# Optimization experiments

Hardware: AMD Instinct MI355X
Metric: run time of the kernel (lower is better)

The kernel has to match this reference:

```python
import jax, jax.numpy as jnp
import numpy as np
from jax import lax


def _quadrature_weights(bw):
    # s2cnn-style Driscoll-Healy quadrature weights over beta, length 2*bw
    j = np.arange(2 * bw)
    k = np.arange(bw)
    theta = np.pi * (2 * j + 1) / (4 * bw)
    s = (np.sin(np.outer(2 * j + 1, 2 * k + 1) * np.pi / (4 * bw)) / (2 * k + 1)).sum(-1)
    return jnp.asarray((2.0 / bw) * np.sin(theta) * s, jnp.float32)


def _conv2d(x, W, b):
    y = lax.conv_general_dilated(x, W, (1, 1), 'SAME',
                                 dimension_numbers=('NCHW', 'OIHW', 'NCHW'))
    return y + b[None, :, None, None]


def setup_inputs() -> dict:
    key = jax.random.key(0)
    ks = jax.random.split(key, 8)
    b, n = 8, 32768
    res_pt, res_r = 32, 8
    inputs = jax.random.normal(ks[0], (b, n, 3), jnp.float32)
    return {
        'inputs': inputs,
        'scale': jnp.float32(3.0),      # max radius covered by radial bins
        'sigma': jnp.float32(0.5),      # gaussian width in grid units
        'A': jnp.float32(1.0),          # splat amplitude
        'inteval_comp': jnp.float32(0.5),
        'res_pt': res_pt,
        'res_r': res_r,
        'W_s2_1': 0.08 * jax.random.normal(ks[1], (32, 8, 3, 3), jnp.float32),
        'b_s2_1': jnp.zeros((32,), jnp.float32),
        'W_s2_2': 0.05 * jax.random.normal(ks[2], (64, 32, 3, 3), jnp.float32),
        'b_s2_2': jnp.zeros((64,), jnp.float32),
        'W_gamma': 0.1 * jax.random.normal(ks[3], (64, 32), jnp.float32),
        'W_c3_1': 0.05 * jax.random.normal(ks[4], (64, 128), jnp.float32),
        'b_c3_1': jnp.zeros((64,), jnp.float32),
        'W_c3_2': 0.05 * jax.random.normal(ks[5], (32, 64), jnp.float32),
        'b_c3_2': jnp.zeros((32,), jnp.float32),
    }


def reference(inputs, scale, sigma, A, inteval_comp, res_pt, res_r,
              W_s2_1, b_s2_1, W_s2_2, b_s2_2, W_gamma,
              W_c3_1, b_c3_1, W_c3_2, b_c3_2):
    b, n, _ = inputs.shape
    # ---- remap: cartesian -> spherical with min-radius clamp (utils.remap) ----
    x, y, z = inputs[..., 0], inputs[..., 1], inputs[..., 2]
    r = jnp.maximum(jnp.sqrt(x * x + y * y + z * z), 0.1)
    theta = jnp.arccos(jnp.clip(z / r, -1.0, 1.0))            # [0, pi]
    phi = jnp.arctan2(y, x) + np.pi                            # [0, 2pi)
    # ---- s2_gridding: gaussian-weighted point -> (theta,phi,r) grid scatter ----
    ct = theta / np.pi * res_pt                                # continuous bin coords
    cp = phi / (2 * np.pi) * res_pt
    cr = r / scale * res_r
    it = jnp.clip(jnp.floor(ct).astype(jnp.int32), 0, res_pt - 1)
    ip = jnp.clip(jnp.floor(cp).astype(jnp.int32), 0, res_pt - 1)
    ir = jnp.clip(jnp.floor(cr).astype(jnp.int32), 0, res_r - 1)
    d2 = ((ct - (it + inteval_comp)) ** 2
          + (cp - (ip + inteval_comp)) ** 2
          + (cr - (ir + inteval_comp)) ** 2)
    w = A * jnp.exp(-d2 / (2.0 * sigma * sigma))               # (b, n)
    vals = jnp.stack([w, w * x, w * y, w * z], axis=-1)        # (b, n, 4)
    bidx = jnp.arange(b, dtype=jnp.int32)[:, None] * jnp.ones((1, n), jnp.int32)
    flat = ((bidx * res_pt + it) * res_pt + ip) * res_r + ir   # (b, n)
    grid = jnp.zeros((b * res_pt * res_pt * res_r, 4), jnp.float32)
    grid = grid.at[flat.reshape(-1)].add(vals.reshape(-1, 4))
    grid = grid.reshape(b, res_pt, res_pt, res_r, 4)
    ft = jnp.transpose(grid[..., 0], (0, 3, 1, 2))             # (b, res_r, res_pt, res_pt)
    # ---- encoder_l1 (s2cnn_equators): S2 convs + gamma lift to SO3 grid ----
    h = jax.nn.relu(_conv2d(ft, W_s2_1, b_s2_1))
    h = jax.nn.relu(_conv2d(h, W_s2_2, b_s2_2))                # (b, 64, res_pt, res_pt)
    ft_grid = jnp.einsum('bcxy,cg->bcxyg', h, W_gamma)         # (b, 64, rp, rp, rp)
    # ---- so3_integrate: quadrature weight over beta, sum alpha/gamma ----
    wq = _quadrature_weights(res_pt // 2)                      # (res_pt,)
    ft_max = jnp.einsum('bcxyg,y->bc', ft_grid, wq)            # (b, 64)
    # ---- broadcast global feature, concat, pointwise conv3d head ----
    ft_max_ = jnp.broadcast_to(ft_max[:, :, None, None, None],
                               (b, ft_grid.shape[1], res_pt, res_pt, res_pt))
    cat = jnp.concatenate([ft_grid, ft_max_], axis=1)          # (b, 128, rp, rp, rp)
    h3 = jax.nn.relu(jnp.einsum('bcxyg,dc->bdxyg', cat, W_c3_1)
                     + b_c3_1[None, :, None, None, None])
    out = (jnp.einsum('bdxyg,ed->bexyg', h3, W_c3_2)
           + b_c3_2[None, :, None, None, None])                # (b, 32, rp, rp, rp)
    ft_g = out.reshape(b, out.shape[1], -1).max(-1)            # (b, 32)
    return (out, ft_g)
```

## Files before the change

### kernel.cpp

```cpp
#include <hip/hip_runtime.h>
#include <math.h>

#define PI_D 3.14159265358979323846
#define PI_F 3.14159265358979323846f

typedef _Float16 half8 __attribute__((ext_vector_type(8)));
typedef _Float16 half2v __attribute__((ext_vector_type(2)));
typedef float floatx4 __attribute__((ext_vector_type(4)));
#define MFMA16(a,b,c) __builtin_amdgcn_mfma_f32_16x16x32_f16(a,b,c,0,0,0)

__global__ void k_scatter(const float* __restrict__ inp,
                          const float* __restrict__ p_scale,
                          const float* __restrict__ p_sigma,
                          const float* __restrict__ p_A,
                          const float* __restrict__ p_ic,
                          float* __restrict__ ft) {
  int i = blockIdx.x * 256 + threadIdx.x;
  float scale = p_scale[0];
  float sigma = p_sigma[0];
  float A     = p_A[0];
  float icomp = p_ic[0];
  int b = i >> 15;
  float x = inp[i*3+0];
  float y = inp[i*3+1];
  float z = inp[i*3+2];
  float r = sqrtf(x*x + y*y + z*z);
  r = fmaxf(r, 0.1f);
  float ctv = fminf(fmaxf(z / r, -1.0f), 1.0f);
  float theta = acosf(ctv);
  float phi = atan2f(y, x) + PI_F;
  float ct = theta * (32.0f / PI_F);
  float cp = phi * (32.0f / (2.0f * PI_F));
  float cr = r / scale * 8.0f;
  int it = (int)floorf(ct); it = min(max(it, 0), 31);
  int ip = (int)floorf(cp); ip = min(max(ip, 0), 31);
  int ir = (int)floorf(cr); ir = min(max(ir, 0), 7);
  float dt = ct - ((float)it + icomp);
  float dp = cp - ((float)ip + icomp);
  float dr = cr - ((float)ir + icomp);
  float d2 = dt*dt + dp*dp + dr*dr;
  float w = A * expf(-d2 / (2.0f * sigma * sigma));
  atomicAdd(&ft[((b*8 + ir)*32 + it)*32 + ip], w);
}

__global__ void k_wq(float* __restrict__ wq) {
  int t = threadIdx.x;
  double jj = 2.0*(double)t + 1.0;
  double theta = PI_D * jj / 64.0;
  double s = 0.0;
  for (int k = 0; k < 16; ++k)
    s += sin(jj * (double)(2*k+1) * PI_D / 64.0) / (double)(2*k+1);
  wq[t] = (float)((2.0/16.0) * sin(theta) * s);
}

__global__ void k_prepV(const float* __restrict__ Wg, const float* __restrict__ Wc31,
                        _Float16* __restrict__ VswH, _Float16* __restrict__ VswL) {
  int flat = blockIdx.x * 256 + threadIdx.x;
  int jj = flat & 7;
  int l  = (flat >> 3) & 63;
  int rest = flat >> 9;
  int ks = rest & 1, mt = rest >> 1;
  int c = ks*32 + (l >> 4)*8 + jj;
  int m = mt*16 + (l & 15);
  int g = m >> 6, d = m & 63;
  float val = Wg[c*32 + g] * Wc31[d*128 + c];
  _Float16 hi = (_Float16)val;
  _Float16 lo = (_Float16)(val - (float)hi);
  VswH[flat] = hi;
  VswL[flat] = lo;
}

__global__ void k_prepW2(const float* __restrict__ Wc32,
                         _Float16* __restrict__ W2swH, _Float16* __restrict__ W2swL) {
  int flat = blockIdx.x * 256 + threadIdx.x;
  int jj = flat & 7;
  int l  = (flat >> 3) & 63;
  int rest = flat >> 9;
  int ks = rest & 1, mt2 = rest >> 1;
  int e = mt2*16 + (l & 15);
  int d = ks*32 + (l >> 4)*8 + jj;
  float val = Wc32[e*64 + d];
  _Float16 hi = (_Float16)val;
  _Float16 lo = (_Float16)(val - (float)hi);
  W2swH[flat] = hi;
  W2swL[flat] = lo;
}

__global__ void k_conv1(const float* __restrict__ ft, const float* __restrict__ W,
                        const float* __restrict__ bias, float* __restrict__ h1) {
  int blk = blockIdx.x;
  int b = blk >> 5, oc = blk & 31;
  __shared__ float Ws[72];
  int t = threadIdx.x;
  if (t < 72) Ws[t] = W[oc*72 + t];
  __syncthreads();
  int x = t >> 5, y = t & 31;
  float acc = bias[oc];
  const float* fb = ft + b*8192;
  for (int ic = 0; ic < 8; ++ic) {
    const float* fc = fb + ic*1024;
    const float* wr = Ws + ic*9;
#pragma unroll
    for (int dx = -1; dx <= 1; ++dx) {
      int xx = x + dx;
      bool okx = ((unsigned)xx < 32u);
#pragma unroll
      for (int dy = -1; dy <= 1; ++dy) {
        int yy = y + dy;
        float v = (okx && ((unsigned)yy < 32u)) ? fc[xx*32 + yy] : 0.f;
        acc = fmaf(v, wr[(dx+1)*3 + (dy+1)], acc);
      }
    }
  }
  h1[(b*32 + oc)*1024 + t] = fmaxf(acc, 0.f);
}

__global__ __launch_bounds__(512) void k_conv2(const float* __restrict__ h1,
                        const float* __restrict__ W,
                        const float* __restrict__ bias, float* __restrict__ h2) {
  int blk = blockIdx.x;
  int b = blk >> 5, q = blk & 31;
  int oc0 = (q >> 1) * 4, xh = q & 1;
  __shared__ float Ws[4*288];
  int t = threadIdx.x;
  for (int idx = t; idx < 4*288; idx += 512) Ws[idx] = W[oc0*288 + idx];
  __syncthreads();
  int x = xh*16 + (t >> 5), y = t & 31;
  float a0 = bias[oc0+0], a1 = bias[oc0+1], a2 = bias[oc0+2], a3 = bias[oc0+3];
  const float* hb = h1 + b*32*1024;
  for (int ic = 0; ic < 32; ++ic) {
    const float* hc = hb + ic*1024;
    const float* w0 = Ws + 0*288 + ic*9;
    const float* w1 = Ws + 1*288 + ic*9;
    const float* w2 = Ws + 2*288 + ic*9;
    const float* w3 = Ws + 3*288 + ic*9;
#pragma unroll
    for (int dx = -1; dx <= 1; ++dx) {
      int xx = x + dx;
      bool okx = ((unsigned)xx < 32u);
#pragma unroll
      for (int dy = -1; dy <= 1; ++dy) {
        int yy = y + dy;
        float v = (okx && ((unsigned)yy < 32u)) ? hc[xx*32 + yy] : 0.f;
        int k = (dx+1)*3 + (dy+1);
        a0 = fmaf(v, w0[k], a0);
        a1 = fmaf(v, w1[k], a1);
        a2 = fmaf(v, w2[k], a2);
        a3 = fmaf(v, w3[k], a3);
      }
    }
  }
  int p = x*32 + y;
  h2[(b*64 + oc0+0)*1024 + p] = fmaxf(a0, 0.f);
  h2[(b*64 + oc0+1)*1024 + p] = fmaxf(a1, 0.f);
  h2[(b*64 + oc0+2)*1024 + p] = fmaxf(a2, 0.f);
  h2[(b*64 + oc0+3)*1024 + p] = fmaxf(a3, 0.f);
}

__global__ void k_reduce(const float* __restrict__ h2, const float* __restrict__ Wg,
                         const float* __restrict__ wq, float* __restrict__ ftmax) {
  int blk = blockIdx.x;
  int b = blk >> 6, c = blk & 63;
  __shared__ float wqs[32];
  __shared__ float red[256];
  int t = threadIdx.x;
  if (t < 32) wqs[t] = wq[t];
  __syncthreads();
  const float* hb = h2 + (b*64 + c)*1024;
  float acc = 0.f;
  for (int i = t; i < 1024; i += 256) acc = fmaf(hb[i], wqs[i & 31], acc);
  red[t] = acc;
  __syncthreads();
  for (int s2 = 128; s2 > 0; s2 >>= 1) {
    if (t < s2) red[t] += red[t + s2];
    __syncthreads();
  }
  if (t == 0) {
    float sg = 0.f;
    for (int g = 0; g < 32; ++g) sg += Wg[c*32 + g];
    ftmax[b*64 + c] = sg * red[0];
  }
}

__global__ __launch_bounds__(512) void k_head(
    const float* __restrict__ h2, const float* __restrict__ ftmax,
    const float* __restrict__ Wc31, const float* __restrict__ bc31,
    const float* __restrict__ bc32,
    const half8* __restrict__ VswH, const half8* __restrict__ VswL,
    const half8* __restrict__ W2swH, const half8* __restrict__ W2swL,
    float* __restrict__ out, float* __restrict__ blockmax) {
  __shared__ __align__(16) _Float16 h3H[512*72];
  __shared__ __align__(16) _Float16 h3L[512*72];
  __shared__ __align__(16) _Float16 h2H[32*72];
  __shared__ __align__(16) _Float16 h2L[32*72];
  __shared__ float Ks[64];
  __shared__ float vbuf2[8*16];
  int blk = blockIdx.x;
  int b = blk >> 5, x = blk & 31;
  int t = threadIdx.x;
  int lane = t & 63, w = t >> 6;
  int n16 = lane & 15, quad = lane >> 4;

  for (int idx = t; idx < 2048; idx += 512) {
    int c = idx & 63, y = idx >> 6;
    float v = h2[(b*64 + c)*1024 + x*32 + y];
    _Float16 hi = (_Float16)v;
    h2H[y*72 + c] = hi;
    h2L[y*72 + c] = (_Float16)(v - (float)hi);
  }
  if (t < 64) {
    float acc = bc31[t];
    for (int c = 0; c < 64; ++c)
      acc = fmaf(Wc31[t*128 + 64 + c], ftmax[b*64 + c], acc);
    Ks[t] = acc;
  }
  __syncthreads();

  half8 bh00, bh01, bh10, bh11, bl00, bl01, bl10, bl11;
  {
    int a00 = (0*16 + n16)*72 + 0*32 + quad*8;
    int a01 = (0*16 + n16)*72 + 1*32 + quad*8;
    int a10 = (1*16 + n16)*72 + 0*32 + quad*8;
    int a11 = (1*16 + n16)*72 + 1*32 + quad*8;
    bh00 = *(const half8*)&h2H[a00];  bl00 = *(const half8*)&h2L[a00];
    bh01 = *(const half8*)&h2H[a01];  bl01 = *(const half8*)&h2L[a01];
    bh10 = *(const half8*)&h2H[a10];  bl10 = *(const half8*)&h2L[a10];
    bh11 = *(const half8*)&h2H[a11];  bl11 = *(const half8*)&h2L[a11];
  }
  int mt2 = w & 1;
  half8 a2h0 = W2swH[(mt2*2 + 0)*64 + lane];
  half8 a2h1 = W2swH[(mt2*2 + 1)*64 + lane];
  half8 a2l0 = W2swL[(mt2*2 + 0)*64 + lane];
  half8 a2l1 = W2swL[(mt2*2 + 1)*64 + lane];
  float bias_e[4];
#pragma unroll
  for (int r = 0; r < 4; ++r) bias_e[r] = bc32[mt2*16 + quad*4 + r];

  float vmax[4] = {-3.4e38f, -3.4e38f, -3.4e38f, -3.4e38f};

  for (int h = 0; h < 2; ++h) {
    if (h) __syncthreads();
    for (int i = 0; i < 8; ++i) {
      int mt = h*64 + w*8 + i;
      half8 ah0 = VswH[(mt*2 + 0)*64 + lane];
      half8 ah1 = VswH[(mt*2 + 1)*64 + lane];
      half8 al0 = VswL[(mt*2 + 0)*64 + lane];
      half8 al1 = VswL[(mt*2 + 1)*64 + lane];
      floatx4 acc0 = {0.f, 0.f, 0.f, 0.f};
      floatx4 acc1 = {0.f, 0.f, 0.f, 0.f};
      acc0 = MFMA16(ah0, bh00, acc0);  acc1 = MFMA16(ah0, bh10, acc1);
      acc0 = MFMA16(ah0, bl00, acc0);  acc1 = MFMA16(ah0, bl10, acc1);
      acc0 = MFMA16(al0, bh00, acc0);  acc1 = MFMA16(al0, bh10, acc1);
      acc0 = MFMA16(ah1, bh01, acc0);  acc1 = MFMA16(ah1, bh11, acc1);
      acc0 = MFMA16(ah1, bl01, acc0);  acc1 = MFMA16(ah1, bl11, acc1);
      acc0 = MFMA16(al1, bh01, acc0);  acc1 = MFMA16(al1, bh11, acc1);
      int g = mt >> 2, gl = g & 15;
      int dbase = (mt & 3)*16 + quad*4;
      float4 kv = *(const float4*)&Ks[dbase];
#pragma unroll
      for (int nt = 0; nt < 2; ++nt) {
        floatx4 a = nt ? acc1 : acc0;
        int y = nt*16 + n16;
        int rowc = y*16 + gl;
        int dsw = (dbase + y*8) & 63;
        float v0 = fmaxf(a[0] + kv.x, 0.f);
        float v1 = fmaxf(a[1] + kv.y, 0.f);
        float v2 = fmaxf(a[2] + kv.z, 0.f);
        float v3 = fmaxf(a[3] + kv.w, 0.f);
        _Float16 c0 = (_Float16)v0, c1 = (_Float16)v1, c2 = (_Float16)v2, c3 = (_Float16)v3;
        half2v hh0 = {c0, c1}, hh1 = {c2, c3};
        half2v ll0 = {(_Float16)(v0 - (float)c0), (_Float16)(v1 - (float)c1)};
        half2v ll1 = {(_Float16)(v2 - (float)c2), (_Float16)(v3 - (float)c3)};
        int base = rowc*72 + dsw;
        *(half2v*)&h3H[base]     = hh0;
        *(half2v*)&h3H[base + 2] = hh1;
        *(half2v*)&h3L[base]     = ll0;
        *(half2v*)&h3L[base + 2] = ll1;
      }
    }
    __syncthreads();
    for (int i = 0; i < 8; ++i) {
      int nt2 = (w >> 1)*8 + i;
      int rowc = nt2*16 + n16;
      floatx4 acc = {0.f, 0.f, 0.f, 0.f};
      {
        int dsw0 = (0*32 + quad*8 + nt2*8) & 63;
        int dsw1 = (1*32 + quad*8 + nt2*8) & 63;
        half8 b2h0 = *(const half8*)&h3H[rowc*72 + dsw0];
        half8 b2l0 = *(const half8*)&h3L[rowc*72 + dsw0];
        half8 b2h1 = *(const half8*)&h3H[rowc*72 + dsw1];
        half8 b2l1 = *(const half8*)&h3L[rowc*72 + dsw1];
        acc = MFMA16(a2h0, b2h0, acc);
        acc = MFMA16(a2h0, b2l0, acc);
        acc = MFMA16(a2l0, b2h0, acc);
        acc = MFMA16(a2h1, b2h1, acc);
        acc = MFMA16(a2h1, b2l1, acc);
        acc = MFMA16(a2l1, b2h1, acc);
      }
      int y = nt2, g = h*16 + n16;
      size_t base = (((size_t)(b*32 + mt2*16 + quad*4))*1024 + (size_t)(x*32 + y))*32 + g;
#pragma unroll
      for (int r = 0; r < 4; ++r) {
        float v = acc[r] + bias_e[r];
        out[base + (size_t)r*32768] = v;
        vmax[r] = fmaxf(vmax[r], v);
      }
    }
  }
#pragma unroll
  for (int m = 1; m < 16; m <<= 1) {
#pragma unroll
    for (int r = 0; r < 4; ++r)
      vmax[r] = fmaxf(vmax[r], __shfl_xor(vmax[r], m, 64));
  }
  if (n16 == 0) {
#pragma unroll
    for (int r = 0; r < 4; ++r) vbuf2[w*16 + quad*4 + r] = vmax[r];
  }
  __syncthreads();
  if (t < 32) {
    int e = t, m2 = e >> 4, el = e & 15;
    float mm = fmaxf(fmaxf(vbuf2[(m2+0)*16 + el], vbuf2[(m2+2)*16 + el]),
                     fmaxf(vbuf2[(m2+4)*16 + el], vbuf2[(m2+6)*16 + el]));
    blockmax[blk*32 + e] = mm;
  }
}

__global__ void k_final(const float* __restrict__ blockmax, float* __restrict__ ftg) {
  int t = threadIdx.x;
  int b = t >> 5, e = t & 31;
  float m = -3.4e38f;
  for (int x = 0; x < 32; ++x) m = fmaxf(m, blockmax[(b*32 + x)*32 + e]);
  ftg[b*32 + e] = m;
}

extern "C" void kernel_launch(void* const* d_in, const int* in_sizes, int n_in,
                              void* d_out, int out_size, void* d_ws, size_t ws_size,
                              hipStream_t stream) {
  const float* inputs = (const float*)d_in[0];
  const float* scale  = (const float*)d_in[1];
  const float* sigma  = (const float*)d_in[2];
  const float* A      = (const float*)d_in[3];
  const float* icmp   = (const float*)d_in[4];
  const float* W1   = (const float*)d_in[7];
  const float* b1   = (const float*)d_in[8];
  const float* W2   = (const float*)d_in[9];
  const float* b2   = (const float*)d_in[10];
  const float* Wg   = (const float*)d_in[11];
  const float* Wc31 = (const float*)d_in[12];
  const float* bc31 = (const float*)d_in[13];
  const float* Wc32 = (const float*)d_in[14];
  const float* bc32 = (const float*)d_in[15];

  float* ws    = (float*)d_ws;
  float* ft    = ws;
  float* h1    = ws + 65536;
  float* h2    = ws + 327680;
  float* ftmax = ws + 851968;
  float* bmax  = ws + 852480;
  float* wq    = ws + 860672;
  _Float16* VswH  = (_Float16*)(ws + 860704);
  _Float16* VswL  = (_Float16*)(ws + 926240);
  _Float16* W2swH = (_Float16*)(ws + 991776);
  _Float16* W2swL = (_Float16*)(ws + 992800);
  float* out   = (float*)d_out;
  float* ftg   = out + 8388608;

  hipMemsetAsync(ft, 0, 65536*sizeof(float), stream);
  k_wq<<<1, 32, 0, stream>>>(wq);
  k_prepV<<<512, 256, 0, stream>>>(Wg, Wc31, VswH, VswL);
  k_prepW2<<<8, 256, 0, stream>>>(Wc32, W2swH, W2swL);
  k_scatter<<<1024, 256, 0, stream>>>(inputs, scale, sigma, A, icmp, ft);
  k_conv1<<<256, 1024, 0, stream>>>(ft, W1, b1, h1);
  k_conv2<<<256, 512, 0, stream>>>(h1, W2, b2, h2);
  k_reduce<<<512, 256, 0, stream>>>(h2, Wg, wq, ftmax);
  k_head<<<256, 512, 0, stream>>>(h2, ftmax, Wc31, bc31, bc32,
                                  (const half8*)VswH, (const half8*)VswL,
                                  (const half8*)W2swH, (const half8*)W2swL,
                                  out, bmax);
  k_final<<<1, 256, 0, stream>>>(bmax, ftg);
}
```

Measured before the change: 179.8 us.

## Fuse all stages into one cooperative persistent kernel with grid syncs

Replaces the memset and nine separate kernel launches with a single cooperative kernel of 256 blocks that runs every stage in sequence, separated by grid-wide barriers. Shared memory is one byte buffer that each stage reinterprets. The goal is to remove per-launch overhead and the idle gaps between dependent small kernels. In exchange, each stage is limited to 256 blocks, so conv1, the scatter and the reduce each do more work per thread. Each grid.sync has its own cost, and the large shared allocation limits occupancy for every phase.

Result: slower. 332.3 us (+84.8%).

```diff
diff --git a/kernel.cpp b/kernel.cpp
--- a/kernel.cpp
+++ b/kernel.cpp
@@ -1,5 +1,8 @@
 #include <hip/hip_runtime.h>
+#include <hip/hip_cooperative_groups.h>
 #include <math.h>
+
+namespace cg = cooperative_groups;
 
 #define PI_D 3.14159265358979323846
 #define PI_F 3.14159265358979323846f
@@ -9,374 +12,369 @@
 typedef float floatx4 __attribute__((ext_vector_type(4)));
 #define MFMA16(a,b,c) __builtin_amdgcn_mfma_f32_16x16x32_f16(a,b,c,0,0,0)
 
-__global__ void k_scatter(const float* __restrict__ inp,
-                          const float* __restrict__ p_scale,
-                          const float* __restrict__ p_sigma,
-                          const float* __restrict__ p_A,
-                          const float* __restrict__ p_ic,
-                          float* __restrict__ ft) {
-  int i = blockIdx.x * 256 + threadIdx.x;
-  float scale = p_scale[0];
-  float sigma = p_sigma[0];
-  float A     = p_A[0];
-  float icomp = p_ic[0];
-  int b = i >> 15;
-  float x = inp[i*3+0];
-  float y = inp[i*3+1];
-  float z = inp[i*3+2];
-  float r = sqrtf(x*x + y*y + z*z);
-  r = fmaxf(r, 0.1f);
-  float ctv = fminf(fmaxf(z / r, -1.0f), 1.0f);
-  float theta = acosf(ctv);
-  float phi = atan2f(y, x) + PI_F;
-  float ct = theta * (32.0f / PI_F);
-  float cp = phi * (32.0f / (2.0f * PI_F));
-  float cr = r / scale * 8.0f;
-  int it = (int)floorf(ct); it = min(max(it, 0), 31);
-  int ip = (int)floorf(cp); ip = min(max(ip, 0), 31);
-  int ir = (int)floorf(cr); ir = min(max(ir, 0), 7);
-  float dt = ct - ((float)it + icomp);
-  float dp = cp - ((float)ip + icomp);
-  float dr = cr - ((float)ir + icomp);
-  float d2 = dt*dt + dp*dp + dr*dr;
-  float w = A * expf(-d2 / (2.0f * sigma * sigma));
-  atomicAdd(&ft[((b*8 + ir)*32 + it)*32 + ip], w);
-}
-
-__global__ void k_wq(float* __restrict__ wq) {
-  int t = threadIdx.x;
-  double jj = 2.0*(double)t + 1.0;
-  double theta = PI_D * jj / 64.0;
-  double s = 0.0;
-  for (int k = 0; k < 16; ++k)
-    s += sin(jj * (double)(2*k+1) * PI_D / 64.0) / (double)(2*k+1);
-  wq[t] = (float)((2.0/16.0) * sin(theta) * s);
-}
-
-__global__ void k_prepV(const float* __restrict__ Wg, const float* __restrict__ Wc31,
-                        _Float16* __restrict__ VswH, _Float16* __restrict__ VswL) {
-  int flat = blockIdx.x * 256 + threadIdx.x;
-  int jj = flat & 7;
-  int l  = (flat >> 3) & 63;
-  int rest = flat >> 9;
-  int ks = rest & 1, mt = rest >> 1;
-  int c = ks*32 + (l >> 4)*8 + jj;
-  int m = mt*16 + (l & 15);
-  int g = m >> 6, d = m & 63;
-  float val = Wg[c*32 + g] * Wc31[d*128 + c];
-  _Float16 hi = (_Float16)val;
-  _Float16 lo = (_Float16)(val - (float)hi);
-  VswH[flat] = hi;
-  VswL[flat] = lo;
-}
-
-__global__ void k_prepW2(const float* __restrict__ Wc32,
-                         _Float16* __restrict__ W2swH, _Float16* __restrict__ W2swL) {
-  int flat = blockIdx.x * 256 + threadIdx.x;
-  int jj = flat & 7;
-  int l  = (flat >> 3) & 63;
-  int rest = flat >> 9;
-  int ks = rest & 1, mt2 = rest >> 1;
-  int e = mt2*16 + (l & 15);
-  int d = ks*32 + (l >> 4)*8 + jj;
-  float val = Wc32[e*64 + d];
-  _Float16 hi = (_Float16)val;
-  _Float16 lo = (_Float16)(val - (float)hi);
-  W2swH[flat] = hi;
-  W2swL[flat] = lo;
-}
-
-__global__ void k_conv1(const float* __restrict__ ft, const float* __restrict__ W,
-                        const float* __restrict__ bias, float* __restrict__ h1) {
-  int blk = blockIdx.x;
-  int b = blk >> 5, oc = blk & 31;
-  __shared__ float Ws[72];
-  int t = threadIdx.x;
-  if (t < 72) Ws[t] = W[oc*72 + t];
-  __syncthreads();
-  int x = t >> 5, y = t & 31;
-  float acc = bias[oc];
-  const float* fb = ft + b*8192;
-  for (int ic = 0; ic < 8; ++ic) {
-    const float* fc = fb + ic*1024;
-    const float* wr = Ws + ic*9;
-#pragma unroll
-    for (int dx = -1; dx <= 1; ++dx) {
-      int xx = x + dx;
-      bool okx = ((unsigned)xx < 32u);
-#pragma unroll
-      for (int dy = -1; dy <= 1; ++dy) {
-        int yy = y + dy;
-        float v = (okx && ((unsigned)yy < 32u)) ? fc[xx*32 + yy] : 0.f;
-        acc = fmaf(v, wr[(dx+1)*3 + (dy+1)], acc);
+struct KParams {
+  const float *inp, *scale, *sigma, *A, *icmp;
+  const float *W1, *b1, *W2, *b2, *Wg, *Wc31, *bc31, *Wc32, *bc32;
+  float *ft, *h1, *h2, *ftmax, *bmax, *wq;
+  _Float16 *VswH, *VswL, *W2swH, *W2swL;
+  float *out, *ftg;
+};
+
+__global__ __launch_bounds__(512, 2) void k_main(KParams p) {
+  __shared__ __align__(16) char smem[157440];
+  cg::grid_group grid = cg::this_grid();
+  const int blk = blockIdx.x;
+  const int t = threadIdx.x;
+
+  {
+    int flat = blk * 512 + t;
+    {
+      int jj = flat & 7;
+      int l  = (flat >> 3) & 63;
+      int rest = flat >> 9;
+      int ks = rest & 1, mt = rest >> 1;
+      int c = ks*32 + (l >> 4)*8 + jj;
+      int m = mt*16 + (l & 15);
+      int g = m >> 6, d = m & 63;
+      float val = p.Wg[c*32 + g] * p.Wc31[d*128 + c];
+      _Float16 hi = (_Float16)val;
+      p.VswH[flat] = hi;
+      p.VswL[flat] = (_Float16)(val - (float)hi);
+    }
+    if (flat < 2048) {
+      int jj = flat & 7;
+      int l  = (flat >> 3) & 63;
+      int rest = flat >> 9;
+      int ks = rest & 1, mt2 = rest >> 1;
+      int e = mt2*16 + (l & 15);
+      int d = ks*32 + (l >> 4)*8 + jj;
+      float val = p.Wc32[e*64 + d];
+      _Float16 hi = (_Float16)val;
+      p.W2swH[flat] = hi;
+      p.W2swL[flat] = (_Float16)(val - (float)hi);
+    }
+    if (flat < 16384) ((float4*)p.ft)[flat] = make_float4(0.f, 0.f, 0.f, 0.f);
+    if (blk == 255 && t < 32) {
+      double jj = 2.0*(double)t + 1.0;
+      double theta = PI_D * jj / 64.0;
+      double s = 0.0;
+      for (int k = 0; k < 16; ++k)
+        s += sin(jj * (double)(2*k+1) * PI_D / 64.0) / (double)(2*k+1);
+      p.wq[t] = (float)((2.0/16.0) * sin(theta) * s);
+    }
+  }
+  grid.sync();
+
+  {
+    float scale = p.scale[0], sigma = p.sigma[0], A = p.A[0], icomp = p.icmp[0];
+#pragma unroll
+    for (int ii = 0; ii < 2; ++ii) {
+      int i = blk * 512 + t + ii * 131072;
+      int b = i >> 15;
+      float x = p.inp[i*3+0];
+      float y = p.inp[i*3+1];
+      float z = p.inp[i*3+2];
+      float r = sqrtf(x*x + y*y + z*z);
+      r = fmaxf(r, 0.1f);
+      float ctv = fminf(fmaxf(z / r, -1.0f), 1.0f);
+      float theta = acosf(ctv);
+      float phi = atan2f(y, x) + PI_F;
+      float ct = theta * (32.0f / PI_F);
+      float cp = phi * (32.0f / (2.0f * PI_F));
+      float cr = r / scale * 8.0f;
+      int it = (int)floorf(ct); it = min(max(it, 0), 31);
+      int ip = (int)floorf(cp); ip = min(max(ip, 0), 31);
+      int ir = (int)floorf(cr); ir = min(max(ir, 0), 7);
+      float dt = ct - ((float)it + icomp);
+      float dp = cp - ((float)ip + icomp);
+      float dr = cr - ((float)ir + icomp);
+      float d2 = dt*dt + dp*dp + dr*dr;
+      float w = A * expf(-d2 / (2.0f * sigma * sigma));
+      atomicAdd(&p.ft[((b*8 + ir)*32 + it)*32 + ip], w);
+    }
+  }
+  grid.sync();
+
+  {
+    int b = blk >> 5, oc = blk & 31;
+    float* Ws = (float*)smem;
+    if (t < 72) Ws[t] = p.W1[oc*72 + t];
+    __syncthreads();
+    const float* fb = p.ft + b*8192;
+    float bias = p.b1[oc];
+#pragma unroll
+    for (int pp = 0; pp < 2; ++pp) {
+      int px = t + pp*512;
+      int x = px >> 5, y = px & 31;
+      float acc = bias;
+      for (int ic = 0; ic < 8; ++ic) {
+        const float* fc = fb + ic*1024;
+        const float* wr = Ws + ic*9;
+#pragma unroll
+        for (int dx = -1; dx <= 1; ++dx) {
+          int xx = x + dx;
+          bool okx = ((unsigned)xx < 32u);
+#pragma unroll
+          for (int dy = -1; dy <= 1; ++dy) {
+            int yy = y + dy;
+            float v = (okx && ((unsigned)yy < 32u)) ? fc[xx*32 + yy] : 0.f;
+            acc = fmaf(v, wr[(dx+1)*3 + (dy+1)], acc);
+          }
+        }
       }
-    }
-  }
-  h1[(b*32 + oc)*1024 + t] = fmaxf(acc, 0.f);
-}
-
-__global__ __launch_bounds__(512) void k_conv2(const float* __restrict__ h1,
-                        const float* __restrict__ W,
-                        const float* __restrict__ bias, float* __restrict__ h2) {
-  int blk = blockIdx.x;
-  int b = blk >> 5, q = blk & 31;
-  int oc0 = (q >> 1) * 4, xh = q & 1;
-  __shared__ float Ws[4*288];
-  int t = threadIdx.x;
-  for (int idx = t; idx < 4*288; idx += 512) Ws[idx] = W[oc0*288 + idx];
-  __syncthreads();
-  int x = xh*16 + (t >> 5), y = t & 31;
-  float a0 = bias[oc0+0], a1 = bias[oc0+1], a2 = bias[oc0+2], a3 = bias[oc0+3];
-  const float* hb = h1 + b*32*1024;
-  for (int ic = 0; ic < 32; ++ic) {
-    const float* hc = hb + ic*1024;
-    const float* w0 = Ws + 0*288 + ic*9;
-    const float* w1 = Ws + 1*288 + ic*9;
-    const float* w2 = Ws + 2*288 + ic*9;
-    const float* w3 = Ws + 3*288 + ic*9;
-#pragma unroll
-    for (int dx = -1; dx <= 1; ++dx) {
-      int xx = x + dx;
-      bool okx = ((unsigned)xx < 32u);
-#pragma unroll
-      for (int dy = -1; dy <= 1; ++dy) {
-        int yy = y + dy;
-        float v = (okx && ((unsigned)yy < 32u)) ? hc[xx*32 + yy] : 0.f;
-        int k = (dx+1)*3 + (dy+1);
-        a0 = fmaf(v, w0[k], a0);
-        a1 = fmaf(v, w1[k], a1);
-        a2 = fmaf(v, w2[k], a2);
-        a3 = fmaf(v, w3[k], a3);
+      p.h1[(b*32 + oc)*1024 + px] = fmaxf(acc, 0.f);
+    }
+  }
+  grid.sync();
+
+  {
+    int b = blk >> 5, q = blk & 31;
+    int oc0 = (q >> 1) * 4, xh = q & 1;
+    float* Ws = (float*)smem;
+    for (int idx = t; idx < 4*288; idx += 512) Ws[idx] = p.W2[oc0*288 + idx];
+    __syncthreads();
+    int x = xh*16 + (t >> 5), y = t & 31;
+    float a0 = p.b2[oc0+0], a1 = p.b2[oc0+1], a2 = p.b2[oc0+2], a3 = p.b2[oc0+3];
+    const float* hb = p.h1 + b*32*1024;
+    for (int ic = 0; ic < 32; ++ic) {
+      const float* hc = hb + ic*1024;
+      const float* w0 = Ws + 0*288 + ic*9;
+      const float* w1 = Ws + 1*288 + ic*9;
+      const float* w2 = Ws + 2*288 + ic*9;
+      const float* w3 = Ws + 3*288 + ic*9;
+#pragma unroll
+      for (int dx = -1; dx <= 1; ++dx) {
+        int xx = x + dx;
+        bool okx = ((unsigned)xx < 32u);
+#pragma unroll
+        for (int dy = -1; dy <= 1; ++dy) {
+          int yy = y + dy;
+          float v = (okx && ((unsigned)yy < 32u)) ? hc[xx*32 + yy] : 0.f;
+          int k = (dx+1)*3 + (dy+1);
+          a0 = fmaf(v, w0[k], a0);
+          a1 = fmaf(v, w1[k], a1);
+          a2 = fmaf(v, w2[k], a2);
+          a3 = fmaf(v, w3[k], a3);
+        }
       }
     }
-  }
-  int p = x*32 + y;
-  h2[(b*64 + oc0+0)*1024 + p] = fmaxf(a0, 0.f);
-  h2[(b*64 + oc0+1)*1024 + p] = fmaxf(a1, 0.f);
-  h2[(b*64 + oc0+2)*1024 + p] = fmaxf(a2, 0.f);
-  h2[(b*64 + oc0+3)*1024 + p] = fmaxf(a3, 0.f);
-}
-
-__global__ void k_reduce(const float* __restrict__ h2, const float* __restrict__ Wg,
-                         const float* __restrict__ wq, float* __restrict__ ftmax) {
-  int blk = blockIdx.x;
-  int b = blk >> 6, c = blk & 63;
-  __shared__ float wqs[32];
-  __shared__ float red[256];
-  int t = threadIdx.x;
-  if (t < 32) wqs[t] = wq[t];
-  __syncthreads();
-  const float* hb = h2 + (b*64 + c)*1024;
-  float acc = 0.f;
-  for (int i = t; i < 1024; i += 256) acc = fmaf(hb[i], wqs[i & 31], acc);
-  red[t] = acc;
-  __syncthreads();
-  for (int s2 = 128; s2 > 0; s2 >>= 1) {
-    if (t < s2) red[t] += red[t + s2];
-    __syncthreads();
-  }
-  if (t == 0) {
-    float sg = 0.f;
-    for (int g = 0; g < 32; ++g) sg += Wg[c*32 + g];
-    ftmax[b*64 + c] = sg * red[0];
-  }
-}
-
-__global__ __launch_bounds__(512) void k_head(
-    const float* __restrict__ h2, const float* __restrict__ ftmax,
-    const float* __restrict__ Wc31, const float* __restrict__ bc31,
-    const float* __restrict__ bc32,
-    const half8* __restrict__ VswH, const half8* __restrict__ VswL,
-    const half8* __restrict__ W2swH, const half8* __restrict__ W2swL,
-    float* __restrict__ out, float* __restrict__ blockmax) {
-  __shared__ __align__(16) _Float16 h3H[512*72];
-  __shared__ __align__(16) _Float16 h3L[512*72];
-  __shared__ __align__(16) _Float16 h2H[32*72];
-  __shared__ __align__(16) _Float16 h2L[32*72];
-  __shared__ float Ks[64];
-  __shared__ float vbuf2[8*16];
-  int blk = blockIdx.x;
-  int b = blk >> 5, x = blk & 31;
-  int t = threadIdx.x;
-  int lane = t & 63, w = t >> 6;
-  int n16 = lane & 15, quad = lane >> 4;
-
-  for (int idx = t; idx < 2048; idx += 512) {
-    int c = idx & 63, y = idx >> 6;
-    float v = h2[(b*64 + c)*1024 + x*32 + y];
-    _Float16 hi = (_Float16)v;
-    h2H[y*72 + c] = hi;
-    h2L[y*72 + c] = (_Float16)(v - (float)hi);
-  }
-  if (t < 64) {
-    float acc = bc31[t];
-    for (int c = 0; c < 64; ++c)
-      acc = fmaf(Wc31[t*128 + 64 + c], ftmax[b*64 + c], acc);
-    Ks[t] = acc;
-  }
-  __syncthreads();
-
-  half8 bh00, bh01, bh10, bh11, bl00, bl01, bl10, bl11;
-  {
-    int a00 = (0*16 + n16)*72 + 0*32 + quad*8;
-    int a01 = (0*16 + n16)*72 + 1*32 + quad*8;
-    int a10 = (1*16 + n16)*72 + 0*32 + quad*8;
-    int a11 = (1*16 + n16)*72 + 1*32 + quad*8;
-    bh00 = *(const half8*)&h2H[a00];  bl00 = *(const half8*)&h2L[a00];
-    bh01 = *(const half8*)&h2H[a01];  bl01 = *(const half8*)&h2L[a01];
-    bh10 = *(const half8*)&h2H[a10];  bl10 = *(const half8*)&h2L[a10];
-    bh11 = *(const half8*)&h2H[a11];  bl11 = *(const half8*)&h2L[a11];
-  }
-  int mt2 = w & 1;
-  half8 a2h0 = W2swH[(mt2*2 + 0)*64 + lane];
-  half8 a2h1 = W2swH[(mt2*2 + 1)*64 + lane];
-  half8 a2l0 = W2swL[(mt2*2 + 0)*64 + lane];
-  half8 a2l1 = W2swL[(mt2*2 + 1)*64 + lane];
-  float bias_e[4];
-#pragma unroll
-  for (int r = 0; r < 4; ++r) bias_e[r] = bc32[mt2*16 + quad*4 + r];
-
-  float vmax[4] = {-3.4e38f, -3.4e38f, -3.4e38f, -3.4e38f};
-
-  for (int h = 0; h < 2; ++h) {
-    if (h) __syncthreads();
-    for (int i = 0; i < 8; ++i) {
-      int mt = h*64 + w*8 + i;
-      half8 ah0 = VswH[(mt*2 + 0)*64 + lane];
-      half8 ah1 = VswH[(mt*2 + 1)*64 + lane];
-      half8 al0 = VswL[(mt*2 + 0)*64 + lane];
-      half8 al1 = VswL[(mt*2 + 1)*64 + lane];
-      floatx4 acc0 = {0.f, 0.f, 0.f, 0.f};
-      floatx4 acc1 = {0.f, 0.f, 0.f, 0.f};
-      acc0 = MFMA16(ah0, bh00, acc0);  acc1 = MFMA16(ah0, bh10, acc1);
-      acc0 = MFMA16(ah0, bl00, acc0);  acc1 = MFMA16(ah0, bl10, acc1);
-      acc0 = MFMA16(al0, bh00, acc0);  acc1 = MFMA16(al0, bh10, acc1);
-      acc0 = MFMA16(ah1, bh01, acc0);  acc1 = MFMA16(ah1, bh11, acc1);
-      acc0 = MFMA16(ah1, bl01, acc0);  acc1 = MFMA16(ah1, bl11, acc1);
-      acc0 = MFMA16(al1, bh01, acc0);  acc1 = MFMA16(al1, bh11, acc1);
-      int g = mt >> 2, gl = g & 15;
-      int dbase = (mt & 3)*16 + quad*4;
-      float4 kv = *(const float4*)&Ks[dbase];
-#pragma unroll
-      for (int nt = 0; nt < 2; ++nt) {
-        floatx4 a = nt ? acc1 : acc0;
-        int y = nt*16 + n16;
-        int rowc = y*16 + gl;
-        int dsw = (dbase + y*8) & 63;
-        float v0 = fmaxf(a[0] + kv.x, 0.f);
-        float v1 = fmaxf(a[1] + kv.y, 0.f);
-        float v2 = fmaxf(a[2] + kv.z, 0.f);
-        float v3 = fmaxf(a[3] + kv.w, 0.f);
-        _Float16 c0 = (_Float16)v0, c1 = (_Float16)v1, c2 = (_Float16)v2, c3 = (_Float16)v3;
-        half2v hh0 = {c0, c1}, hh1 = {c2, c3};
-        half2v ll0 = {(_Float16)(v0 - (float)c0), (_Float16)(v1 - (float)c1)};
-        half2v ll1 = {(_Float16)(v2 - (float)c2), (_Float16)(v3 - (float)c3)};
-        int base = rowc*72 + dsw;
-        *(half2v*)&h3H[base]     = hh0;
-        *(half2v*)&h3H[base + 2] = hh1;
-        *(half2v*)&h3L[base]     = ll0;
-        *(half2v*)&h3L[base + 2] = ll1;
+    int pp = x*32 + y;
+    p.h2[(b*64 + oc0+0)*1024 + pp] = fmaxf(a0, 0.f);
+    p.h2[(b*64 + oc0+1)*1024 + pp] = fmaxf(a1, 0.f);
+    p.h2[(b*64 + oc0+2)*1024 + pp] = fmaxf(a2, 0.f);
+    p.h2[(b*64 + oc0+3)*1024 + pp] = fmaxf(a3, 0.f);
+  }
+  grid.sync();
+
+  {
+    float* wqs = (float*)smem;
+    float* red = (float*)smem + 32;
+    int half = t >> 8;
+    int tt = t & 255;
+    int pair = blk*2 + half;
+    int b = pair >> 6, c = pair & 63;
+    if (t < 32) wqs[t] = p.wq[t];
+    __syncthreads();
+    const float* hb = p.h2 + (b*64 + c)*1024;
+    float acc = 0.f;
+    for (int i = tt; i < 1024; i += 256) acc = fmaf(hb[i], wqs[i & 31], acc);
+    red[half*256 + tt] = acc;
+    __syncthreads();
+    for (int s2 = 128; s2 > 0; s2 >>= 1) {
+      if (tt < s2) red[half*256 + tt] += red[half*256 + tt + s2];
+      __syncthreads();
+    }
+    if (tt == 0) {
+      float sg = 0.f;
+      for (int g = 0; g < 32; ++g) sg += p.Wg[c*32 + g];
+      p.ftmax[b*64 + c] = sg * red[half*256];
+    }
+  }
+  grid.sync();
+
+  {
+    _Float16* h3H = (_Float16*)smem;
+    _Float16* h3L = (_Float16*)(smem + 73728);
+    _Float16* h2H = (_Float16*)(smem + 147456);
+    _Float16* h2L = (_Float16*)(smem + 152064);
+    float* Ks     = (float*)(smem + 156672);
+    float* vbuf2  = (float*)(smem + 156928);
+    const half8* VswH  = (const half8*)p.VswH;
+    const half8* VswL  = (const half8*)p.VswL;
+    const half8* W2swH = (const half8*)p.W2swH;
+    const half8* W2swL = (const half8*)p.W2swL;
+
+    int b = blk >> 5, x = blk & 31;
+    int lane = t & 63, w = t >> 6;
+    int n16 = lane & 15, quad = lane >> 4;
+
+    for (int idx = t; idx < 2048; idx += 512) {
+      int c = idx & 63, y = idx >> 6;
+      float v = p.h2[(b*64 + c)*1024 + x*32 + y];
+      _Float16 hi = (_Float16)v;
+      h2H[y*72 + c] = hi;
+      h2L[y*72 + c] = (_Float16)(v - (float)hi);
+    }
+    if (t < 64) {
+      float acc = p.bc31[t];
+      for (int c = 0; c < 64; ++c)
+        acc = fmaf(p.Wc31[t*128 + 64 + c], p.ftmax[b*64 + c], acc);
+      Ks[t] = acc;
+    }
+    __syncthreads();
+
+    half8 bh00, bh01, bh10, bh11, bl00, bl01, bl10, bl11;
+    {
+      int a00 = (0*16 + n16)*72 + 0*32 + quad*8;
+      int a01 = (0*16 + n16)*72 + 1*32 + quad*8;
+      int a10 = (1*16 + n16)*72 + 0*32 + quad*8;
+      int a11 = (1*16 + n16)*72 + 1*32 + quad*8;
+      bh00 = *(const half8*)&h2H[a00];  bl00 = *(const half8*)&h2L[a00];
+      bh01 = *(const half8*)&h2H[a01];  bl01 = *(const half8*)&h2L[a01];
+      bh10 = *(const half8*)&h2H[a10];  bl10 = *(const half8*)&h2L[a10];
+      bh11 = *(const half8*)&h2H[a11];  bl11 = *(const half8*)&h2L[a11];
+    }
+    int mt2 = w & 1;
+    half8 a2h0 = W2swH[(mt2*2 + 0)*64 + lane];
+    half8 a2h1 = W2swH[(mt2*2 + 1)*64 + lane];
+    half8 a2l0 = W2swL[(mt2*2 + 0)*64 + lane];
+    half8 a2l1 = W2swL[(mt2*2 + 1)*64 + lane];
+    float bias_e[4];
+#pragma unroll
+    for (int r = 0; r < 4; ++r) bias_e[r] = p.bc32[mt2*16 + quad*4 + r];
+
+    float vmax[4] = {-3.4e38f, -3.4e38f, -3.4e38f, -3.4e38f};
+
+    for (int h = 0; h < 2; ++h) {
+      if (h) __syncthreads();
+      for (int i = 0; i < 8; ++i) {
+        int mt = h*64 + w*8 + i;
+        half8 ah0 = VswH[(mt*2 + 0)*64 + lane];
+        half8 ah1 = VswH[(mt*2 + 1)*64 + lane];
+        half8 al0 = VswL[(mt*2 + 0)*64 + lane];
+        half8 al1 = VswL[(mt*2 + 1)*64 + lane];
+        floatx4 acc0 = {0.f, 0.f, 0.f, 0.f};
+        floatx4 acc1 = {0.f, 0.f, 0.f, 0.f};
+        acc0 = MFMA16(ah0, bh00, acc0);  acc1 = MFMA16(ah0, bh10, acc1);
+        acc0 = MFMA16(ah0, bl00, acc0);  acc1 = MFMA16(ah0, bl10, acc1);
+        acc0 = MFMA16(al0, bh00, acc0);  acc1 = MFMA16(al0, bh10, acc1);
+        acc0 = MFMA16(ah1, bh01, acc0);  acc1 = MFMA16(ah1, bh11, acc1);
+        acc0 = MFMA16(ah1, bl01, acc0);  acc1 = MFMA16(ah1, bl11, acc1);
+        acc0 = MFMA16(al1, bh01, acc0);  acc1 = MFMA16(al1, bh11, acc1);
+        int g = mt >> 2, gl = g & 15;
+        int dbase = (mt & 3)*16 + quad*4;
+        float4 kv = *(const float4*)&Ks[dbase];
+#pragma unroll
+        for (int nt = 0; nt < 2; ++nt) {
+          floatx4 a = nt ? acc1 : acc0;
+          int y = nt*16 + n16;
+          int rowc = y*16 + gl;
+          int dsw = (dbase + y*8) & 63;
+          float v0 = fmaxf(a[0] + kv.x, 0.f);
+          float v1 = fmaxf(a[1] + kv.y, 0.f);
+          float v2 = fmaxf(a[2] + kv.z, 0.f);
+          float v3 = fmaxf(a[3] + kv.w, 0.f);
+          _Float16 c0 = (_Float16)v0, c1 = (_Float16)v1, c2 = (_Float16)v2, c3 = (_Float16)v3;
+          half2v hh0 = {c0, c1}, hh1 = {c2, c3};
+          half2v ll0 = {(_Float16)(v0 - (float)c0), (_Float16)(v1 - (float)c1)};
+          half2v ll1 = {(_Float16)(v2 - (float)c2), (_Float16)(v3 - (float)c3)};
+          int base = rowc*72 + dsw;
+          *(half2v*)&h3H[base]     = hh0;
+          *(half2v*)&h3H[base + 2] = hh1;
+          *(half2v*)&h3L[base]     = ll0;
+          *(half2v*)&h3L[base + 2] = ll1;
+        }
       }
-    }
-    __syncthreads();
-    for (int i = 0; i < 8; ++i) {
-      int nt2 = (w >> 1)*8 + i;
-      int rowc = nt2*16 + n16;
-      floatx4 acc = {0.f, 0.f, 0.f, 0.f};
-      {
-        int dsw0 = (0*32 + quad*8 + nt2*8) & 63;
-        int dsw1 = (1*32 + quad*8 + nt2*8) & 63;
-        half8 b2h0 = *(const half8*)&h3H[rowc*72 + dsw0];
-        half8 b2l0 = *(const half8*)&h3L[rowc*72 + dsw0];
-        half8 b2h1 = *(const half8*)&h3H[rowc*72 + dsw1];
-        half8 b2l1 = *(const half8*)&h3L[rowc*72 + dsw1];
-        acc = MFMA16(a2h0, b2h0, acc);
-        acc = MFMA16(a2h0, b2l0, acc);
-        acc = MFMA16(a2l0, b2h0, acc);
-        acc = MFMA16(a2h1, b2h1, acc);
-        acc = MFMA16(a2h1, b2l1, acc);
-        acc = MFMA16(a2l1, b2h1, acc);
+      __syncthreads();
+      for (int i = 0; i < 8; ++i) {
+        int nt2 = (w >> 1)*8 + i;
+        int rowc = nt2*16 + n16;
+        floatx4 acc = {0.f, 0.f, 0.f, 0.f};
+        {
+          int dsw0 = (0*32 + quad*8 + nt2*8) & 63;
+          int dsw1 = (1*32 + quad*8 + nt2*8) & 63;
+          half8 b2h0 = *(const half8*)&h3H[rowc*72 + dsw0];
+          half8 b2l0 = *(const half8*)&h3L[rowc*72 + dsw0];
+          half8 b2h1 = *(const half8*)&h3H[rowc*72 + dsw1];
+          half8 b2l1 = *(const half8*)&h3L[rowc*72 + dsw1];
+          acc = MFMA16(a2h0, b2h0, acc);
+          acc = MFMA16(a2h0, b2l0, acc);
+          acc = MFMA16(a2l0, b2h0, acc);
+          acc = MFMA16(a2h1, b2h1, acc);
+          acc = MFMA16(a2h1, b2l1, acc);
+          acc = MFMA16(a2l1, b2h1, acc);
+        }
+        int y = nt2, g = h*16 + n16;
+        size_t base = (((size_t)(b*32 + mt2*16 + quad*4))*1024 + (size_t)(x*32 + y))*32 + g;
+#pragma unroll
+        for (int r = 0; r < 4; ++r) {
+          float v = acc[r] + bias_e[r];
+          p.out[base + (size_t)r*32768] = v;
+          vmax[r] = fmaxf(vmax[r], v);
+        }
       }
-      int y = nt2, g = h*16 + n16;
-      size_t base = (((size_t)(b*32 + mt2*16 + quad*4))*1024 + (size_t)(x*32 + y))*32 + g;
-#pragma unroll
-      for (int r = 0; r < 4; ++r) {
-        float v = acc[r] + bias_e[r];
-        out[base + (size_t)r*32768] = v;
-        vmax[r] = fmaxf(vmax[r], v);
-      }
-    }
-  }
-#pragma unroll
-  for (int m = 1; m < 16; m <<= 1) {
-#pragma unroll
-    for (int r = 0; r < 4; ++r)
-      vmax[r] = fmaxf(vmax[r], __shfl_xor(vmax[r], m, 64));
-  }
-  if (n16 == 0) {
-#pragma unroll
-    for (int r = 0; r < 4; ++r) vbuf2[w*16 + quad*4 + r] = vmax[r];
-  }
-  __syncthreads();
-  if (t < 32) {
-    int e = t, m2 = e >> 4, el = e & 15;
-    float mm = fmaxf(fmaxf(vbuf2[(m2+0)*16 + el], vbuf2[(m2+2)*16 + el]),
-                     fmaxf(vbuf2[(m2+4)*16 + el], vbuf2[(m2+6)*16 + el]));
-    blockmax[blk*32 + e] = mm;
-  }
-}
-
-__global__ void k_final(const float* __restrict__ blockmax, float* __restrict__ ftg) {
-  int t = threadIdx.x;
-  int b = t >> 5, e = t & 31;
-  float m = -3.4e38f;
-  for (int x = 0; x < 32; ++x) m = fmaxf(m, blockmax[(b*32 + x)*32 + e]);
-  ftg[b*32 + e] = m;
+    }
+#pragma unroll
+    for (int m = 1; m < 16; m <<= 1) {
+#pragma unroll
+      for (int r = 0; r < 4; ++r)
+        vmax[r] = fmaxf(vmax[r], __shfl_xor(vmax[r], m, 64));
+    }
+    if (n16 == 0) {
+#pragma unroll
+      for (int r = 0; r < 4; ++r) vbuf2[w*16 + quad*4 + r] = vmax[r];
+    }
+    __syncthreads();
+    if (t < 32) {
+      int e = t, m2 = e >> 4, el = e & 15;
+      float mm = fmaxf(fmaxf(vbuf2[(m2+0)*16 + el], vbuf2[(m2+2)*16 + el]),
+                       fmaxf(vbuf2[(m2+4)*16 + el], vbuf2[(m2+6)*16 + el]));
+      p.bmax[blk*32 + e] = mm;
+    }
+  }
+  grid.sync();
+
+  if (blk == 0 && t < 256) {
+    int b = t >> 5, e = t & 31;
+    float m = -3.4e38f;
+    for (int x = 0; x < 32; ++x) m = fmaxf(m, p.bmax[(b*32 + x)*32 + e]);
+    p.ftg[b*32 + e] = m;
+  }
 }
 
 extern "C" void kernel_launch(void* const* d_in, const int* in_sizes, int n_in,
                               void* d_out, int out_size, void* d_ws, size_t ws_size,
                               hipStream_t stream) {
-  const float* inputs = (const float*)d_in[0];
-  const float* scale  = (const float*)d_in[1];
-  const float* sigma  = (const float*)d_in[2];
-  const float* A      = (const float*)d_in[3];
-  const float* icmp   = (const float*)d_in[4];
-  const float* W1   = (const float*)d_in[7];
-  const float* b1   = (const float*)d_in[8];
-  const float* W2   = (const float*)d_in[9];
-  const float* b2   = (const float*)d_in[10];
-  const float* Wg   = (const float*)d_in[11];
-  const float* Wc31 = (const float*)d_in[12];
-  const float* bc31 = (const float*)d_in[13];
-  const float* Wc32 = (const float*)d_in[14];
-  const float* bc32 = (const float*)d_in[15];
-
-  float* ws    = (float*)d_ws;
-  float* ft    = ws;
-  float* h1    = ws + 65536;
-  float* h2    = ws + 327680;
-  float* ftmax = ws + 851968;
-  float* bmax  = ws + 852480;
-  float* wq    = ws + 860672;
-  _Float16* VswH  = (_Float16*)(ws + 860704);
-  _Float16* VswL  = (_Float16*)(ws + 926240);
-  _Float16* W2swH = (_Float16*)(ws + 991776);
-  _Float16* W2swL = (_Float16*)(ws + 992800);
-  float* out   = (float*)d_out;
-  float* ftg   = out + 8388608;
-
-  hipMemsetAsync(ft, 0, 65536*sizeof(float), stream);
-  k_wq<<<1, 32, 0, stream>>>(wq);
-  k_prepV<<<512, 256, 0, stream>>>(Wg, Wc31, VswH, VswL);
-  k_prepW2<<<8, 256, 0, stream>>>(Wc32, W2swH, W2swL);
-  k_scatter<<<1024, 256, 0, stream>>>(inputs, scale, sigma, A, icmp, ft);
-  k_conv1<<<256, 1024, 0, stream>>>(ft, W1, b1, h1);
-  k_conv2<<<256, 512, 0, stream>>>(h1, W2, b2, h2);
-  k_reduce<<<512, 256, 0, stream>>>(h2, Wg, wq, ftmax);
-  k_head<<<256, 512, 0, stream>>>(h2, ftmax, Wc31, bc31, bc32,
-                                  (const half8*)VswH, (const half8*)VswL,
-                                  (const half8*)W2swH, (const half8*)W2swL,
-                                  out, bmax);
-  k_final<<<1, 256, 0, stream>>>(bmax, ftg);
+  float* ws = (float*)d_ws;
+  KParams prm;
+  prm.inp   = (const float*)d_in[0];
+  prm.scale = (const float*)d_in[1];
+  prm.sigma = (const float*)d_in[2];
+  prm.A     = (const float*)d_in[3];
+  prm.icmp  = (const float*)d_in[4];
+  prm.W1   = (const float*)d_in[7];
+  prm.b1   = (const float*)d_in[8];
+  prm.W2   = (const float*)d_in[9];
+  prm.b2   = (const float*)d_in[10];
+  prm.Wg   = (const float*)d_in[11];
+  prm.Wc31 = (const float*)d_in[12];
+  prm.bc31 = (const float*)d_in[13];
+  prm.Wc32 = (const float*)d_in[14];
+  prm.bc32 = (const float*)d_in[15];
+
+  prm.ft    = ws;
+  prm.h1    = ws + 65536;
+  prm.h2    = ws + 327680;
+  prm.ftmax = ws + 851968;
+  prm.bmax  = ws + 852480;
+  prm.wq    = ws + 860672;
+  prm.VswH  = (_Float16*)(ws + 860704);
+  prm.VswL  = (_Float16*)(ws + 926240);
+  prm.W2swH = (_Float16*)(ws + 991776);
+  prm.W2swL = (_Float16*)(ws + 992800);
+  prm.out   = (float*)d_out;
+  prm.ftg   = prm.out + 8388608;
+
+  void* kargs[] = { (void*)&prm };
+  hipLaunchCooperativeKernel((void*)k_main, dim3(256), dim3(512), kargs, 0, stream);
 }
```
